# Kernel optimization log

Measured on AMD Instinct MI355X. Metric: run time of the kernel, lower is better.

Reference implementation:

```python
import jax, jax.numpy as jnp
import numpy as np

N, C, G = 50000, 30, 1000   # cells, classes, genes
E = 800000                   # edges
OUT = 8                      # GATv2 out channels, heads=1


def setup_inputs() -> dict:
    key = jax.random.key(0)
    ks = jax.random.split(key, 12)
    X = jax.random.normal(ks[0], (N, G), dtype=jnp.float32)
    Mu = jax.random.normal(ks[1], (C, G), dtype=jnp.float32)
    Var = jax.random.uniform(ks[2], (C, G), dtype=jnp.float32) + 0.5  # strictly positive
    edge_index = jax.random.randint(ks[3], (2, E), 0, N, dtype=jnp.int64)
    # learned params
    W = 0.01 * jax.random.normal(ks[4], (N, C), dtype=jnp.float32)   # torch init zeros; small noise for nontrivial P
    S = jnp.ones((N, 1), dtype=jnp.float32)
    sc = 1.0 / np.sqrt(G)
    Wl = sc * jax.random.normal(ks[5], (OUT, G), dtype=jnp.float32)  # lin_l weight
    bl = jnp.zeros((OUT,), dtype=jnp.float32)
    Wr = sc * jax.random.normal(ks[6], (OUT, G), dtype=jnp.float32)  # lin_r weight
    br = jnp.zeros((OUT,), dtype=jnp.float32)
    att = jax.random.normal(ks[7], (OUT,), dtype=jnp.float32) / np.sqrt(OUT)
    return {"X": X, "Mu": Mu, "Var": Var, "edge_index": edge_index,
            "W": W, "S": S, "Wl": Wl, "bl": bl, "Wr": Wr, "br": br, "att": att}


def reference(X, Mu, Var, edge_index, W, S, Wl, bl, Wr, br, att):
    n = X.shape[0]
    P = jax.nn.softmax(W, axis=1)                       # [N,C]
    # Gaussian log-likelihood term. Expand (X - Mu*S)^2/Var summed over genes:
    invVar = 1.0 / Var                                  # [C,G]
    A = (X * X) @ invVar.T                              # [N,C]  sum X^2/Var
    B = X @ (Mu * invVar).T                             # [N,C]  sum X*Mu/Var
    D = jnp.sum(Mu * Mu * invVar, axis=1)               # [C]    sum Mu^2/Var
    Fmat = -0.5 * (A - 2.0 * S * B + (S * S) * D[None, :])  # [N,C]
    ll_prot = jnp.sum(P * Fmat) / n

    # GATv2 attention (heads=1, add_self_loops=False)
    x_l = X @ Wl.T + bl                                 # [N,8] source transform
    x_r = X @ Wr.T + br                                 # [N,8] target transform
    src, dst = edge_index[0], edge_index[1]
    m = jax.nn.leaky_relu(x_l[src] + x_r[dst], negative_slope=0.2)  # [E,8]
    e = m @ att                                         # [E]
    # edge-softmax grouped by destination node
    emax = jax.ops.segment_max(e, dst, num_segments=n)  # [N]
    e_exp = jnp.exp(e - emax[dst])                      # [E]
    denom = jax.ops.segment_sum(e_exp, dst, num_segments=n)  # [N]
    alpha = e_exp / (denom[dst] + 1e-16)                # [E]

    ce_space = -jnp.sum(P[src] * alpha[:, None] * jnp.log(P[dst] + 1e-8)) / n
    return ll_prot, ce_space, P
```

## Files before the change

kernel.cpp:

```cpp
#include <hip/hip_runtime.h>
#include <math.h>

#define N_CELLS 50000
#define C_CLS   30
#define G_GENES 1000
#define E_EDGES 800000
#define KPAD    1024

typedef __attribute__((ext_vector_type(8))) short bf16x8;
typedef __attribute__((ext_vector_type(4))) float f32x4;

__device__ __forceinline__ unsigned f2bf_u(float f) {
    unsigned u = __float_as_uint(f);
    return (u + 0x7fffu + ((u >> 16) & 1u)) >> 16;
}
__device__ __forceinline__ unsigned pack2(float lo, float hi) {
    return f2bf_u(lo) | (f2bf_u(hi) << 16);
}

__device__ __forceinline__ float lrelu02(float v) { return v > 0.f ? v : 0.2f * v; }

__device__ __forceinline__ float dp4(int4 a, int4 b) {
    const unsigned* ua = (const unsigned*)&a;
    const unsigned* ub = (const unsigned*)&b;
    float s = 0.f;
#pragma unroll
    for (int i = 0; i < 4; i++) {
        float al = __uint_as_float(ua[i] << 16);
        float ah = __uint_as_float(ua[i] & 0xffff0000u);
        float bl = __uint_as_float(ub[i] << 16);
        float bh = __uint_as_float(ub[i] & 0xffff0000u);
        s += al * bl + ah * bh;
    }
    return s;
}

__global__ void prep_kernel(const float* __restrict__ Mu, const float* __restrict__ Var,
                            const float* __restrict__ Wl, const float* __restrict__ Wr,
                            unsigned short* __restrict__ CoefB, float* __restrict__ Dvec,
                            float* __restrict__ denom, float* __restrict__ out) {
    const int r = blockIdx.x;
    const int t = threadIdx.x;
    __shared__ float red[256];
    float dacc = 0.f;
    for (int g = t; g < KPAD; g += 256) {
        float v = 0.f;
        if (g < G_GENES) {
            if (r < 30) {
                float iv = 1.0f / Var[r * G_GENES + g];
                float mu = Mu[r * G_GENES + g];
                v = iv;
                dacc += mu * mu * iv;
            } else if (r >= 32) {
                int i = r - 32;
                if (i < 30)      v = Mu[i * G_GENES + g] / Var[i * G_GENES + g];
                else if (i < 38) v = Wl[(i - 30) * G_GENES + g];
                else if (i < 46) v = Wr[(i - 38) * G_GENES + g];
            }
        }
        CoefB[r * KPAD + g] = (unsigned short)f2bf_u(v);
    }
    for (int i = blockIdx.x * 256 + t; i < N_CELLS; i += 80 * 256) denom[i] = 0.f;
    if (r == 31 && t < 2) out[t] = 0.f;

    if (r < 30) {
        red[t] = dacc;
        __syncthreads();
        for (int s = 128; s > 0; s >>= 1) {
            if (t < s) red[t] += red[t + s];
            __syncthreads();
        }
        if (t == 0) Dvec[r] = red[0];
    }
}

__global__ __launch_bounds__(256, 4) void main_rows_kernel(
    const float* __restrict__ X, const float* __restrict__ W,
    const float* __restrict__ S, const float* __restrict__ bl,
    const float* __restrict__ br, const unsigned short* __restrict__ CoefB,
    const float* __restrict__ Dvec,
    float* __restrict__ out,
    unsigned short* __restrict__ Pb, unsigned short* __restrict__ Lb,
    float* __restrict__ xl, float* __restrict__ xr)
{
    __shared__ __align__(16) unsigned short Ct[80 * 72];

    const int t    = threadIdx.x;
    const int w    = t >> 6;
    const int l    = t & 63;
    const int l15  = l & 15;
    const int quad = l >> 4;
    const int wavebase = blockIdx.x * 64 + w * 16;
    const bool valid = (wavebase < N_CELLS);
    const float* __restrict__ xrow = X + (size_t)(wavebase + l15) * G_GENES;

    f32x4 acc[5];
#pragma unroll
    for (int i = 0; i < 5; i++) acc[i] = (f32x4){0.f, 0.f, 0.f, 0.f};

    for (int kt = 0; kt < KPAD; kt += 64) {
        __syncthreads();
        for (int u = t; u < 640; u += 256) {
            int row = u >> 3;
            int kk  = (u & 7) * 8;
            *(int4*)&Ct[row * 72 + kk] = *(const int4*)&CoefB[row * KPAD + kt + kk];
        }
        __syncthreads();
#pragma unroll
        for (int ks = 0; ks < 2; ks++) {
            const int k0 = kt + ks * 32 + quad * 8;
            float4 f0 = make_float4(0.f, 0.f, 0.f, 0.f);
            float4 f1 = make_float4(0.f, 0.f, 0.f, 0.f);
            if (valid && k0 < G_GENES) {
                f0 = *(const float4*)&xrow[k0];
                f1 = *(const float4*)&xrow[k0 + 4];
            }
            union { unsigned u[4]; bf16x8 v; } ua, u2;
            ua.u[0] = pack2(f0.x, f0.y);
            ua.u[1] = pack2(f0.z, f0.w);
            ua.u[2] = pack2(f1.x, f1.y);
            ua.u[3] = pack2(f1.z, f1.w);
            u2.u[0] = pack2(f0.x * f0.x, f0.y * f0.y);
            u2.u[1] = pack2(f0.z * f0.z, f0.w * f0.w);
            u2.u[2] = pack2(f1.x * f1.x, f1.y * f1.y);
            u2.u[3] = pack2(f1.z * f1.z, f1.w * f1.w);
#pragma unroll
            for (int nt = 0; nt < 5; nt++) {
                bf16x8 b = *(const bf16x8*)&Ct[(nt * 16 + l15) * 72 + ks * 32 + quad * 8];
                acc[nt] = __builtin_amdgcn_mfma_f32_16x16x32_bf16(
                    nt < 2 ? u2.v : ua.v, b, acc[nt], 0, 0, 0);
            }
        }
    }

    if (!valid) return;

    const int rbase = wavebase + quad * 4;
    const bool c2ok = (l15 < 14);
    const float d0 = Dvec[l15];
    const float d1 = c2ok ? Dvec[16 + l15] : 0.f;
    float llacc = 0.f;
#pragma unroll
    for (int r = 0; r < 4; r++) {
        const int row = rbase + r;
        float w0 = W[(size_t)row * 30 + l15];
        float w1 = c2ok ? W[(size_t)row * 30 + 16 + l15] : -1e30f;
        float m = fmaxf(w0, w1);
#pragma unroll
        for (int mm = 1; mm < 16; mm <<= 1) m = fmaxf(m, __shfl_xor(m, mm, 64));
        float e0 = __expf(w0 - m);
        float e1 = c2ok ? __expf(w1 - m) : 0.f;
        float s = e0 + e1;
#pragma unroll
        for (int mm = 1; mm < 16; mm <<= 1) s += __shfl_xor(s, mm, 64);
        float inv = 1.0f / s;
        float p0 = e0 * inv, p1 = e1 * inv;
        float Sn = S[row], Sn2 = Sn * Sn;
        float F0 = -0.5f * (acc[0][r] - 2.0f * Sn * acc[2][r] + Sn2 * d0);
        float F1 = -0.5f * (acc[1][r] - 2.0f * Sn * acc[3][r] + Sn2 * d1);
        float lp = p0 * F0 + (c2ok ? p1 * F1 : 0.f);
#pragma unroll
        for (int mm = 1; mm < 16; mm <<= 1) lp += __shfl_xor(lp, mm, 64);
        llacc += lp;

        out[2 + (size_t)row * 30 + l15] = p0;
        float lg0 = __logf(p0 + 1e-8f);
        Pb[(size_t)row * 32 + l15] = (unsigned short)f2bf_u(p0);
        Lb[(size_t)row * 32 + l15] = (unsigned short)f2bf_u(lg0);
        if (c2ok) {
            out[2 + (size_t)row * 30 + 16 + l15] = p1;
            float lg1 = __logf(p1 + 1e-8f);
            Pb[(size_t)row * 32 + 16 + l15] = (unsigned short)f2bf_u(p1);
            Lb[(size_t)row * 32 + 16 + l15] = (unsigned short)f2bf_u(lg1);
        } else {
            Pb[(size_t)row * 32 + 16 + l15] = 0;
            Lb[(size_t)row * 32 + 16 + l15] = 0;
        }
        if (l15 >= 14)                xl[(size_t)row * 8 + (l15 - 14)] = acc[3][r] + bl[l15 - 14];
        else if (l15 < 6)             xl[(size_t)row * 8 + (l15 + 2)]  = acc[4][r] + bl[l15 + 2];
        if (l15 >= 6 && l15 < 14)     xr[(size_t)row * 8 + (l15 - 6)]  = acc[4][r] + br[l15 - 6];
    }
    llacc += __shfl_xor(llacc, 16, 64);
    llacc += __shfl_xor(llacc, 32, 64);
    if (l == 0) atomicAdd(&out[0], llacc * (1.0f / N_CELLS));
}

__global__ void edge_passA(const int* __restrict__ ei, const float* __restrict__ xl,
                           const float* __restrict__ xr, const float* __restrict__ att,
                           float* __restrict__ evals, float* __restrict__ denom) {
    int e = blockIdx.x * 256 + threadIdx.x;
    if (e >= E_EDGES) return;
    int src = ei[e];
    int dst = ei[E_EDGES + e];
    const float4* lp = (const float4*)&xl[(size_t)src * 8];
    const float4* rp = (const float4*)&xr[(size_t)dst * 8];
    float4 l0 = lp[0], l1 = lp[1];
    float4 r0 = rp[0], r1 = rp[1];
    float ev = 0.f;
    ev += lrelu02(l0.x + r0.x) * att[0];
    ev += lrelu02(l0.y + r0.y) * att[1];
    ev += lrelu02(l0.z + r0.z) * att[2];
    ev += lrelu02(l0.w + r0.w) * att[3];
    ev += lrelu02(l1.x + r1.x) * att[4];
    ev += lrelu02(l1.y + r1.y) * att[5];
    ev += lrelu02(l1.z + r1.z) * att[6];
    ev += lrelu02(l1.w + r1.w) * att[7];
    float p = __expf(ev);
    evals[e] = p;
    atomicAdd(&denom[dst], p);
}

__global__ __launch_bounds__(256) void edge_passB(
    const int* __restrict__ ei, const float* __restrict__ evals,
    const float* __restrict__ denom, const unsigned short* __restrict__ Pb,
    const unsigned short* __restrict__ Lb, float* __restrict__ out) {
    const int t = threadIdx.x;
    const int e = blockIdx.x * 256 + t;
    int src = ei[e];
    int dst = ei[E_EDGES + e];
    float alpha = evals[e] / (denom[dst] + 1e-16f);
    const int4* ps = (const int4*)&Pb[(size_t)src * 32];
    const int4* ld = (const int4*)&Lb[(size_t)dst * 32];
    int4 a0 = ps[0], a1 = ps[1], a2 = ps[2], a3 = ps[3];
    int4 b0 = ld[0], b1 = ld[1], b2 = ld[2], b3 = ld[3];
    float dot = dp4(a0, b0) + dp4(a1, b1) + dp4(a2, b2) + dp4(a3, b3);
    float contrib = -alpha * dot;

    for (int m = 1; m < 64; m <<= 1) contrib += __shfl_xor(contrib, m, 64);
    __shared__ float wsum[4];
    if ((t & 63) == 0) wsum[t >> 6] = contrib;
    __syncthreads();
    if (t == 0)
        atomicAdd(&out[1], (wsum[0] + wsum[1] + wsum[2] + wsum[3]) * (1.0f / N_CELLS));
}

extern "C" void kernel_launch(void* const* d_in, const int* in_sizes, int n_in,
                              void* d_out, int out_size, void* d_ws, size_t ws_size,
                              hipStream_t stream) {
    const float* X   = (const float*)d_in[0];
    const float* Mu  = (const float*)d_in[1];
    const float* Var = (const float*)d_in[2];
    const int*   ei  = (const int*)d_in[3];
    const float* W   = (const float*)d_in[4];
    const float* S   = (const float*)d_in[5];
    const float* Wl  = (const float*)d_in[6];
    const float* bl  = (const float*)d_in[7];
    const float* Wr  = (const float*)d_in[8];
    const float* br  = (const float*)d_in[9];
    const float* att = (const float*)d_in[10];

    float* out = (float*)d_out;

    float* wsf = (float*)d_ws;
    unsigned short* CoefB = (unsigned short*)wsf;
    float* Dvec  = wsf + 40960;
    unsigned short* Pb = (unsigned short*)(wsf + 40992);
    unsigned short* Lb = (unsigned short*)(wsf + 840992);
    float* xl    = wsf + 1640992;
    float* xr    = wsf + 2040992;
    float* evals = wsf + 2440992;
    float* denom = wsf + 3240992;

    prep_kernel<<<80, 256, 0, stream>>>(Mu, Var, Wl, Wr, CoefB, Dvec, denom, out);
    main_rows_kernel<<<(N_CELLS + 63) / 64, 256, 0, stream>>>(
        X, W, S, bl, br, CoefB, Dvec, out, Pb, Lb, xl, xr);
    edge_passA<<<(E_EDGES + 255) / 256, 256, 0, stream>>>(ei, xl, xr, att, evals, denom);
    edge_passB<<<E_EDGES / 256, 256, 0, stream>>>(ei, evals, denom, Pb, Lb, out);
}
```

Baseline: 456.6 us.

## Prefetch X tiles in GEMM loop, replicate denom atomics, store edge exps in bf16

The main row kernel now loads the next 64-wide K slice of X into registers while the current slice is converted and fed to MFMA, which should hide global load latency. Edge pass A spreads its atomic adds over four replicated denominator arrays keyed by block index to reduce atomic contention. A new small kernel sums the replicas. Edge exponentials are stored as bf16 to halve that traffic, and the same rounded value is added to the denominator so alpha stays consistent, at some precision cost.

Result: no change. 452.1 us (-1.0%).

```diff
diff --git a/kernel.cpp b/kernel.cpp
--- a/kernel.cpp
+++ b/kernel.cpp
@@ -6,6 +6,7 @@
 #define G_GENES 1000
 #define E_EDGES 800000
 #define KPAD    1024
+#define NREP    4
 
 typedef __attribute__((ext_vector_type(8))) short bf16x8;
 typedef __attribute__((ext_vector_type(4))) float f32x4;
@@ -16,6 +17,9 @@
 }
 __device__ __forceinline__ unsigned pack2(float lo, float hi) {
     return f2bf_u(lo) | (f2bf_u(hi) << 16);
+}
+__device__ __forceinline__ float bf2f(unsigned short u) {
+    return __uint_as_float(((unsigned)u) << 16);
 }
 
 __device__ __forceinline__ float lrelu02(float v) { return v > 0.f ? v : 0.2f * v; }
@@ -38,7 +42,7 @@
 __global__ void prep_kernel(const float* __restrict__ Mu, const float* __restrict__ Var,
                             const float* __restrict__ Wl, const float* __restrict__ Wr,
                             unsigned short* __restrict__ CoefB, float* __restrict__ Dvec,
-                            float* __restrict__ denom, float* __restrict__ out) {
+                            float* __restrict__ denom4, float* __restrict__ out) {
     const int r = blockIdx.x;
     const int t = threadIdx.x;
     __shared__ float red[256];
@@ -60,7 +64,7 @@
         }
         CoefB[r * KPAD + g] = (unsigned short)f2bf_u(v);
     }
-    for (int i = blockIdx.x * 256 + t; i < N_CELLS; i += 80 * 256) denom[i] = 0.f;
+    for (int i = blockIdx.x * 256 + t; i < N_CELLS * NREP; i += 80 * 256) denom4[i] = 0.f;
     if (r == 31 && t < 2) out[t] = 0.f;
 
     if (r < 30) {
@@ -90,6 +94,7 @@
     const int l    = t & 63;
     const int l15  = l & 15;
     const int quad = l >> 4;
+    const int k0q  = quad * 8;
     const int wavebase = blockIdx.x * 64 + w * 16;
     const bool valid = (wavebase < N_CELLS);
     const float* __restrict__ xrow = X + (size_t)(wavebase + l15) * G_GENES;
@@ -97,6 +102,14 @@
     f32x4 acc[5];
 #pragma unroll
     for (int i = 0; i < 5; i++) acc[i] = (f32x4){0.f, 0.f, 0.f, 0.f};
+
+    float4 c0a = make_float4(0,0,0,0), c0b = c0a, c1a = c0a, c1b = c0a;
+    if (valid) {
+        c0a = *(const float4*)&xrow[k0q];
+        c0b = *(const float4*)&xrow[k0q + 4];
+        c1a = *(const float4*)&xrow[32 + k0q];
+        c1b = *(const float4*)&xrow[32 + k0q + 4];
+    }
 
     for (int kt = 0; kt < KPAD; kt += 64) {
         __syncthreads();
@@ -106,31 +119,47 @@
             *(int4*)&Ct[row * 72 + kk] = *(const int4*)&CoefB[row * KPAD + kt + kk];
         }
         __syncthreads();
-#pragma unroll
-        for (int ks = 0; ks < 2; ks++) {
-            const int k0 = kt + ks * 32 + quad * 8;
-            float4 f0 = make_float4(0.f, 0.f, 0.f, 0.f);
-            float4 f1 = make_float4(0.f, 0.f, 0.f, 0.f);
-            if (valid && k0 < G_GENES) {
-                f0 = *(const float4*)&xrow[k0];
-                f1 = *(const float4*)&xrow[k0 + 4];
+
+        float4 n0a = make_float4(0,0,0,0), n0b = n0a, n1a = n0a, n1b = n0a;
+        const int ktn = kt + 64;
+        if (valid && ktn < KPAD) {
+            const int ka = ktn + k0q;
+            n0a = *(const float4*)&xrow[ka];
+            n0b = *(const float4*)&xrow[ka + 4];
+            const int kb = ktn + 32 + k0q;
+            if (kb < G_GENES) {
+                n1a = *(const float4*)&xrow[kb];
+                n1b = *(const float4*)&xrow[kb + 4];
             }
-            union { unsigned u[4]; bf16x8 v; } ua, u2;
-            ua.u[0] = pack2(f0.x, f0.y);
-            ua.u[1] = pack2(f0.z, f0.w);
-            ua.u[2] = pack2(f1.x, f1.y);
-            ua.u[3] = pack2(f1.z, f1.w);
-            u2.u[0] = pack2(f0.x * f0.x, f0.y * f0.y);
-            u2.u[1] = pack2(f0.z * f0.z, f0.w * f0.w);
-            u2.u[2] = pack2(f1.x * f1.x, f1.y * f1.y);
-            u2.u[3] = pack2(f1.z * f1.z, f1.w * f1.w);
-#pragma unroll
-            for (int nt = 0; nt < 5; nt++) {
-                bf16x8 b = *(const bf16x8*)&Ct[(nt * 16 + l15) * 72 + ks * 32 + quad * 8];
-                acc[nt] = __builtin_amdgcn_mfma_f32_16x16x32_bf16(
-                    nt < 2 ? u2.v : ua.v, b, acc[nt], 0, 0, 0);
-            }
-        }
+        }
+
+        union { unsigned u[4]; bf16x8 v; } ua, u2;
+        ua.u[0] = pack2(c0a.x, c0a.y); ua.u[1] = pack2(c0a.z, c0a.w);
+        ua.u[2] = pack2(c0b.x, c0b.y); ua.u[3] = pack2(c0b.z, c0b.w);
+        u2.u[0] = pack2(c0a.x * c0a.x, c0a.y * c0a.y);
+        u2.u[1] = pack2(c0a.z * c0a.z, c0a.w * c0a.w);
+        u2.u[2] = pack2(c0b.x * c0b.x, c0b.y * c0b.y);
+        u2.u[3] = pack2(c0b.z * c0b.z, c0b.w * c0b.w);
+#pragma unroll
+        for (int nt = 0; nt < 5; nt++) {
+            bf16x8 b = *(const bf16x8*)&Ct[(nt * 16 + l15) * 72 + k0q];
+            acc[nt] = __builtin_amdgcn_mfma_f32_16x16x32_bf16(
+                nt < 2 ? u2.v : ua.v, b, acc[nt], 0, 0, 0);
+        }
+        ua.u[0] = pack2(c1a.x, c1a.y); ua.u[1] = pack2(c1a.z, c1a.w);
+        ua.u[2] = pack2(c1b.x, c1b.y); ua.u[3] = pack2(c1b.z, c1b.w);
+        u2.u[0] = pack2(c1a.x * c1a.x, c1a.y * c1a.y);
+        u2.u[1] = pack2(c1a.z * c1a.z, c1a.w * c1a.w);
+        u2.u[2] = pack2(c1b.x * c1b.x, c1b.y * c1b.y);
+        u2.u[3] = pack2(c1b.z * c1b.z, c1b.w * c1b.w);
+#pragma unroll
+        for (int nt = 0; nt < 5; nt++) {
+            bf16x8 b = *(const bf16x8*)&Ct[(nt * 16 + l15) * 72 + 32 + k0q];
+            acc[nt] = __builtin_amdgcn_mfma_f32_16x16x32_bf16(
+                nt < 2 ? u2.v : ua.v, b, acc[nt], 0, 0, 0);
+        }
+
+        c0a = n0a; c0b = n0b; c1a = n1a; c1b = n1b;
     }
 
     if (!valid) return;
@@ -187,7 +216,7 @@
 
 __global__ void edge_passA(const int* __restrict__ ei, const float* __restrict__ xl,
                            const float* __restrict__ xr, const float* __restrict__ att,
-                           float* __restrict__ evals, float* __restrict__ denom) {
+                           unsigned short* __restrict__ evalsB, float* __restrict__ denom4) {
     int e = blockIdx.x * 256 + threadIdx.x;
     if (e >= E_EDGES) return;
     int src = ei[e];
@@ -206,19 +235,26 @@
     ev += lrelu02(l1.z + r1.z) * att[6];
     ev += lrelu02(l1.w + r1.w) * att[7];
     float p = __expf(ev);
-    evals[e] = p;
-    atomicAdd(&denom[dst], p);
+    evalsB[e] = (unsigned short)f2bf_u(p);
+    atomicAdd(&denom4[(blockIdx.x & (NREP - 1)) * N_CELLS + dst], bf2f(f2bf_u(p)));
+}
+
+__global__ void reduce_denom(const float* __restrict__ denom4, float* __restrict__ denom) {
+    int i = blockIdx.x * 256 + threadIdx.x;
+    if (i < N_CELLS)
+        denom[i] = (denom4[i] + denom4[N_CELLS + i]) +
+                   (denom4[2 * N_CELLS + i] + denom4[3 * N_CELLS + i]);
 }
 
 __global__ __launch_bounds__(256) void edge_passB(
-    const int* __restrict__ ei, const float* __restrict__ evals,
+    const int* __restrict__ ei, const unsigned short* __restrict__ evalsB,
     const float* __restrict__ denom, const unsigned short* __restrict__ Pb,
     const unsigned short* __restrict__ Lb, float* __restrict__ out) {
     const int t = threadIdx.x;
     const int e = blockIdx.x * 256 + t;
     int src = ei[e];
     int dst = ei[E_EDGES + e];
-    float alpha = evals[e] / (denom[dst] + 1e-16f);
+    float alpha = bf2f(evalsB[e]) / (denom[dst] + 1e-16f);
     const int4* ps = (const int4*)&Pb[(size_t)src * 32];
     const int4* ld = (const int4*)&Lb[(size_t)dst * 32];
     int4 a0 = ps[0], a1 = ps[1], a2 = ps[2], a3 = ps[3];
@@ -252,18 +288,20 @@
     float* out = (float*)d_out;
 
     float* wsf = (float*)d_ws;
-    unsigned short* CoefB = (unsigned short*)wsf;
-    float* Dvec  = wsf + 40960;
-    unsigned short* Pb = (unsigned short*)(wsf + 40992);
-    unsigned short* Lb = (unsigned short*)(wsf + 840992);
-    float* xl    = wsf + 1640992;
-    float* xr    = wsf + 2040992;
-    float* evals = wsf + 2440992;
-    float* denom = wsf + 3240992;
-
-    prep_kernel<<<80, 256, 0, stream>>>(Mu, Var, Wl, Wr, CoefB, Dvec, denom, out);
+    unsigned short* CoefB  = (unsigned short*)wsf;
+    float* Dvec            = wsf + 40960;
+    unsigned short* Pb     = (unsigned short*)(wsf + 40992);
+    unsigned short* Lb     = (unsigned short*)(wsf + 840992);
+    float* xl              = wsf + 1640992;
+    float* xr              = wsf + 2040992;
+    unsigned short* evalsB = (unsigned short*)(wsf + 2440992);
+    float* denom           = wsf + 2840992;
+    float* denom4          = wsf + 2890992;
+
+    prep_kernel<<<80, 256, 0, stream>>>(Mu, Var, Wl, Wr, CoefB, Dvec, denom4, out);
     main_rows_kernel<<<(N_CELLS + 63) / 64, 256, 0, stream>>>(
         X, W, S, bl, br, CoefB, Dvec, out, Pb, Lb, xl, xr);
-    edge_passA<<<(E_EDGES + 255) / 256, 256, 0, stream>>>(ei, xl, xr, att, evals, denom);
-    edge_passB<<<E_EDGES / 256, 256, 0, stream>>>(ei, evals, denom, Pb, Lb, out);
-}
+    edge_passA<<<(E_EDGES + 255) / 256, 256, 0, stream>>>(ei, xl, xr, att, evalsB, denom4);
+    reduce_denom<<<(N_CELLS + 255) / 256, 256, 0, stream>>>(denom4, denom);
+    edge_passB<<<E_EDGES / 256, 256, 0, stream>>>(ei, evalsB, denom, Pb, Lb, out);
+}
```
